# Kernel optimization log

Hardware: AMD Instinct MI355X
Metric: run time of the kernel (lower is better)

The kernel has to match this reference:

```python
import jax, jax.numpy as jnp
import numpy as np
import math

DIM = 768
NUM_HEADS = 16
PERHEAD = DIM // NUM_HEADS  # 48
B, T = 4, 2048


def setup_inputs() -> dict:
    key = jax.random.key(0)
    k_x, k_wi, k_bi, k_wo, k_bo = jax.random.split(key, 5)
    s_in = 1.0 / math.sqrt(DIM)
    return {
        "x": jax.random.normal(k_x, (B, T, DIM), dtype=jnp.float32),
        # linear_in: y = x @ w_in + b_in, w_in: (DIM, 3*DIM)
        "w_in": jax.random.uniform(k_wi, (DIM, 3 * DIM), jnp.float32, -s_in, s_in),
        "b_in": jax.random.uniform(k_bi, (3 * DIM,), jnp.float32, -s_in, s_in),
        "w_out": jax.random.uniform(k_wo, (DIM, DIM), jnp.float32, -s_in, s_in),
        "b_out": jax.random.uniform(k_bo, (DIM,), jnp.float32, -s_in, s_in),
    }


def reference(x, w_in, b_in, w_out, b_out):
    bs, tok, _ = x.shape
    qkv = x @ w_in + b_in                                   # (B, T, 3*DIM)
    # Faithful to torch: reshape to (B, T, H, 3*ph), move heads, chunk last dim.
    qkv = qkv.reshape(bs, tok, NUM_HEADS, 3 * PERHEAD)
    qkv = jnp.transpose(qkv, (0, 2, 1, 3))                  # (B, H, T, 3*ph)
    q, k, v = jnp.split(qkv, 3, axis=-1)                    # each (B, H, T, ph)
    scale = 1.0 / math.sqrt(PERHEAD)
    scores = jnp.einsum("bhqd,bhkd->bhqk", q, k) * scale    # (B, H, T, T)
    attn = jax.nn.softmax(scores, axis=-1)
    # dropout p=0.0 (eval) -> identity
    out = jnp.einsum("bhqk,bhkd->bhqd", attn, v)            # (B, H, T, ph)
    out = jnp.transpose(out, (0, 2, 1, 3)).reshape(bs, tok, DIM)
    return out @ w_out + b_out
```

## Files before the change

kernel.cpp:

```cpp
#include <hip/hip_runtime.h>
#include <hip/hip_bf16.h>
#include <math.h>

typedef __attribute__((ext_vector_type(8))) short short8;
typedef __attribute__((ext_vector_type(4))) float floatx4;
typedef __hip_bfloat16 bf16;

#define DIM 768
#define NHEADS 16
#define PH 48
#define VROWS 49
#define BATCH 4
#define SEQ 2048
#define MTOK (BATCH*SEQ)
#define NQKV (3*DIM)
#define NQK (2*DIM)
#define LOG2E 1.44269504088896f
#define CFAC (0.14433756729740643f * LOG2E)

#define NB_CAST   6144
#define NB_TWIN   1728
#define NB_TWOUT  576
#define NB_MISC   140

__device__ __forceinline__ void cp16(void* dst, const void* src) {
    *(float4*)dst = *(const float4*)src;
}
__device__ __forceinline__ unsigned short f2us(float v) {
    bf16 b = __float2bfloat16(v);
    return *(unsigned short*)&b;
}
__device__ __forceinline__ float us2f(unsigned short u) {
    bf16 b = *(bf16*)&u;
    return __bfloat162float(b);
}
__device__ __forceinline__ void gload_lds16(const bf16* g, bf16* l) {
    __builtin_amdgcn_global_load_lds(
        (const __attribute__((address_space(1))) unsigned int*)g,
        (__attribute__((address_space(3))) unsigned int*)l, 16, 0, 0);
}
__device__ __forceinline__ bool sniff_f32(const unsigned short* __restrict__ x) {
    float v = us2f(x[threadIdx.x & 63]);
    int bad = !(fabsf(v) < 64.0f);
    return __any(bad) != 0;
}

__global__ __launch_bounds__(256) void prep_all(
    const void* __restrict__ x, const void* __restrict__ w_in,
    const void* __restrict__ w_out, const void* __restrict__ bin,
    const void* __restrict__ bout,
    bf16* __restrict__ xb, bf16* __restrict__ winT, bf16* __restrict__ woutT,
    float* __restrict__ bi, float* __restrict__ bo, bf16* __restrict__ Vt)
{
    __shared__ bf16 tile[32][33];
    const int bid = blockIdx.x, tid = threadIdx.x;
    const bool f32 = sniff_f32((const unsigned short*)x);

    if (bid < NB_CAST) {
        int i = bid * 256 + tid;
        if (f32) {
            float4 v = ((const float4*)x)[i];
            ushort4 o;
            o.x = f2us(v.x); o.y = f2us(v.y); o.z = f2us(v.z); o.w = f2us(v.w);
            ((ushort4*)xb)[i] = o;
        } else {
            ((ushort4*)xb)[i] = ((const ushort4*)x)[i];
        }
    } else if (bid < NB_CAST + NB_TWIN + NB_TWOUT) {
        const void* in; bf16* out; int R, C, tt;
        if (bid < NB_CAST + NB_TWIN) {
            in = w_in; out = winT; R = DIM; C = NQKV; tt = bid - NB_CAST;
        } else {
            in = w_out; out = woutT; R = DIM; C = DIM; tt = bid - NB_CAST - NB_TWIN;
        }
        int ctiles = C / 32;
        int c0 = (tt % ctiles) * 32, r0 = (tt / ctiles) * 32;
        int tx = tid & 31, ty = tid >> 5;
#pragma unroll
        for (int j = 0; j < 4; j++) {
            size_t idx = (size_t)(r0 + ty + 8*j) * C + c0 + tx;
            float v = f32 ? ((const float*)in)[idx]
                          : us2f(((const unsigned short*)in)[idx]);
            tile[ty + 8*j][tx] = __float2bfloat16(v);
        }
        __syncthreads();
#pragma unroll
        for (int j = 0; j < 4; j++)
            out[(size_t)(c0 + ty + 8*j) * R + r0 + tx] = tile[tx][ty + 8*j];
    } else {
        int t = (bid - (NB_CAST + NB_TWIN + NB_TWOUT)) * 256 + tid;
        if (t < NQKV) {
            bi[t] = f32 ? ((const float*)bin)[t] : us2f(((const unsigned short*)bin)[t]);
        } else if (t < NQKV + DIM) {
            int j = t - NQKV;
            bo[j] = f32 ? ((const float*)bout)[j] : us2f(((const unsigned short*)bout)[j]);
        } else {
            int k = t - (NQKV + DIM);
            int bh = k >> 9, pos = (k & 511) * 4;
            bf16* dst = Vt + ((size_t)bh * VROWS + 48) * SEQ + pos;
            ushort4 ones;
            ones.x = ones.y = ones.z = ones.w = f2us(1.0f);
            *(ushort4*)dst = ones;
        }
    }
}

template<int N, int MODE, int TM>
__global__ __launch_bounds__(256) void gemm_bias(
    const bf16* __restrict__ A, const bf16* __restrict__ BT,
    const float* __restrict__ bias, void* __restrict__ C0, bf16* __restrict__ Vt,
    const unsigned short* __restrict__ xraw)
{
    constexpr int K = 768;
    constexpr int MI = TM / 32;
    constexpr int TS = TM * 32;
    constexpr int BS = 128 * 32;
    __shared__ __align__(16) bf16 smem[2 * TS + 2 * BS];
    bf16* As0 = smem;
    bf16* As1 = smem + TS;
    bf16* Bs0 = smem + 2 * TS;
    bf16* Bs1 = smem + 2 * TS + BS;
    const bool out_f32 = (MODE == 2) && sniff_f32(xraw);
    const int tid = threadIdx.x;
    const int id = blockIdx.x;
    constexpr int NMB = MTOK / TM;
    const int m0 = (id % NMB) * TM, n0 = (id / NMB) * 128;
    const int w = tid >> 6, lane = tid & 63, lq = lane >> 4, ln = lane & 15;
    const int wr = w & 1, wc = w >> 1;

    const int ssw = ((lane >> 2) ^ (lane >> 4)) & 3;
    const int cm = (lane & 3) ^ ssw;
    const int rlB0 = w * 32 + (lane >> 2), rlB1 = rlB0 + 16;
    const int rlA  = (TM == 128) ? rlB0 : (w * 16 + (lane >> 2));
    const bf16* gA0 = A + (size_t)(m0 + rlA) * K + cm * 8;
    const bf16* gA1 = A + (size_t)(m0 + rlA + ((TM == 128) ? 16 : 0)) * K + cm * 8;
    const bf16* gB0 = BT + (size_t)(n0 + rlB0) * K + cm * 8;
    const bf16* gB1 = BT + (size_t)(n0 + rlB1) * K + cm * 8;
    bf16* lA0 = As0 + ((TM == 128) ? (w * 32) * 32 : (w * 16) * 32);
    bf16* lA1 = As0 + (w * 32 + 16) * 32;
    bf16* lB0 = Bs0 + (w * 32) * 32;
    bf16* lB1 = Bs0 + (w * 32 + 16) * 32;

    const int rsw = (ln ^ (ln >> 2)) & 3;
    const int rchunk = (lq ^ rsw) * 8;

    floatx4 zero4 = {0.f, 0.f, 0.f, 0.f};
    floatx4 acc[MI][4];
#pragma unroll
    for (int mi = 0; mi < MI; mi++)
#pragma unroll
        for (int nj = 0; nj < 4; nj++) acc[mi][nj] = zero4;

    for (int k0 = 0; k0 < K; k0 += 64) {
        gload_lds16(gA0,      lA0);
        gload_lds16(gA0 + 32, lA0 + TS);
        if constexpr (TM == 128) {
            gload_lds16(gA1,      lA1);
            gload_lds16(gA1 + 32, lA1 + TS);
        }
        gload_lds16(gB0,      lB0);
        gload_lds16(gB0 + 32, lB0 + BS);
        gload_lds16(gB1,      lB1);
        gload_lds16(gB1 + 32, lB1 + BS);
        gA0 += 64; gA1 += 64; gB0 += 64; gB1 += 64;
        __syncthreads();

#pragma unroll
        for (int kk = 0; kk < 2; kk++) {
            const bf16* Asub = kk ? As1 : As0;
            const bf16* Bsub = kk ? Bs1 : Bs0;
            short8 a[MI], b[4];
#pragma unroll
            for (int mi = 0; mi < MI; mi++)
                a[mi] = *(const short8*)&Asub[(wr * (TM/2) + 16 * mi + ln) * 32 + rchunk];
#pragma unroll
            for (int nj = 0; nj < 4; nj++)
                b[nj] = *(const short8*)&Bsub[(wc * 64 + 16 * nj + ln) * 32 + rchunk];
#pragma unroll
            for (int mi = 0; mi < MI; mi++)
#pragma unroll
                for (int nj = 0; nj < 4; nj++)
                    acc[mi][nj] = __builtin_amdgcn_mfma_f32_16x16x32_bf16(
                        a[mi], b[nj], acc[mi][nj], 0, 0, 0);
        }
        __syncthreads();
    }
    bf16 (*VLs)[136] = (bf16(*)[136])smem;

#pragma unroll
    for (int nj = 0; nj < 4; nj++) {
        int n = n0 + wc * 64 + 16 * nj + ln;
        float bv = bias[n];
        if (MODE == 2) {
#pragma unroll
            for (int mi = 0; mi < MI; mi++)
#pragma unroll
                for (int i = 0; i < 4; i++) {
                    size_t off = (size_t)(m0 + wr * (TM/2) + 16 * mi + 4 * lq + i) * N + n;
                    float val = acc[mi][nj][i] + bv;
                    if (out_f32) ((float*)C0)[off] = val;
                    else         ((bf16*)C0)[off] = __float2bfloat16(val);
                }
        } else {
            int h = n / 144, r = n - 144 * h;
            if (r < 96) {
                float sc = (r < 48) ? CFAC : 1.0f;
#pragma unroll
                for (int mi = 0; mi < MI; mi++)
#pragma unroll
                    for (int i = 0; i < 4; i++) {
                        size_t off = (size_t)(m0 + wr * (TM/2) + 16 * mi + 4 * lq + i) * NQK
                                     + h * 96 + r;
                        ((bf16*)C0)[off] = __float2bfloat16((acc[mi][nj][i] + bv) * sc);
                    }
            } else {
                int d = r - 96;
#pragma unroll
                for (int mi = 0; mi < MI; mi++)
#pragma unroll
                    for (int i = 0; i < 4; i++)
                        VLs[d][wr * 64 + 32 * (mi >> 1) + 8 * lq + 4 * (mi & 1) + i] =
                            __float2bfloat16(acc[mi][nj][i] + bv);
            }
        }
    }

    if (MODE == 1) {
        __syncthreads();
        const int bidx = m0 >> 11, tok0 = m0 & 2047;
#pragma unroll
        for (int s = 0; s < 3; s++) {
            int idx = tid + 256 * s;
            int d = idx >> 4, ch = idx & 15;
            int h = (n0 + 31 - d) / 144;
            int n = 144 * h + 96 + d;
            if (n >= n0 && n < n0 + 128) {
                bf16* dst = Vt + ((size_t)(bidx * NHEADS + h) * VROWS + d) * SEQ
                            + tok0 + ch * 8;
                *(float4*)dst = *(const float4*)&VLs[d][ch * 8];
            }
        }
    }
}

__global__ __launch_bounds__(256, 2) void attn_fused(
    const bf16* __restrict__ QK, const bf16* __restrict__ Vt, bf16* __restrict__ O)
{
    __shared__ bf16 Ks[2][64][72];
    __shared__ bf16 VsT[2][64][72];

    const int tid = threadIdx.x;
    const int id = blockIdx.x;
    const int g = id & 63, qt = id >> 6;
    const int h = g & 15, b = g >> 4;
    const int w = tid >> 6, lane = tid & 63, lq = lane >> 4, ln = lane & 15;
    const size_t rowbase = (size_t)b * SEQ;
    const int q0 = qt * 256;
    const int hoff = h * 96;
    const bf16* Vth = Vt + (size_t)(b * NHEADS + h) * VROWS * SEQ;

    const bf16 bzero = __float2bfloat16(0.f);
    for (int idx = tid; idx < 2048; idx += 256) {
        int bb = idx >> 10, r = (idx >> 4) & 63, c = idx & 15;
        Ks[bb][r][48 + c] = bzero;
    }

    short8 qa0[4], qa1[4];
    short8 zero8 = {0, 0, 0, 0, 0, 0, 0, 0};
#pragma unroll
    for (int f = 0; f < 4; f++) {
        const bf16* qrow = QK + (rowbase + q0 + 64*f + 16*w + ln) * NQK + hoff;
        qa0[f] = *(const short8*)(qrow + lq * 8);
        qa1[f] = (lq < 2) ? *(const short8*)(qrow + 32 + lq * 8) : zero8;
    }

    const int kr0a = tid / 6, kc0a = tid % 6;
    const int kr1a = (tid + 256) / 6, kc1a = (tid + 256) % 6;
    const char* kg0 = (const char*)(QK + (rowbase + kr0a) * NQK + hoff + 48) + kc0a * 16;
    const char* kg1 = (const char*)(QK + (rowbase + kr1a) * NQK + hoff + 48) + kc1a * 16;
    bf16* kd0 = &Ks[0][kr0a][kc0a * 8];
    bf16* kd1 = &Ks[0][kr1a & 63][kc1a * 8];
    const bool kact = (tid < 128);
    const int vr0 = tid >> 3, vc0 = tid & 7;
    const char* vg0 = (const char*)(Vth + (size_t)vr0 * SEQ) + vc0 * 16;
    const char* vg1 = (const char*)(Vth + (size_t)(32 + vr0) * SEQ) + vc0 * 16;
    bf16* vd0 = &VsT[0][vr0][vc0 * 8];
    bf16* vd1 = &VsT[0][32 + vr0][vc0 * 8];
    const bool vact = (tid < 128);
    const ptrdiff_t KADV = (ptrdiff_t)64 * NQK * 2;
    const ptrdiff_t VADV = 128;
    const int BOFF = 64 * 72;

    floatx4 zero4 = {0.f, 0.f, 0.f, 0.f};
    floatx4 o[4][3];
    float dsum[4] = {0.f, 0.f, 0.f, 0.f};
#pragma unroll
    for (int f = 0; f < 4; f++)
#pragma unroll
        for (int nt = 0; nt < 3; nt++) o[f][nt] = zero4;

    float4 rk0, rk1, rv0, rv1;
    rk0 = *(const float4*)kg0;
    if (kact) rk1 = *(const float4*)kg1;
    rv0 = *(const float4*)vg0;
    if (vact) rv1 = *(const float4*)vg1;
    kg0 += KADV; kg1 += KADV; vg0 += VADV; vg1 += VADV;
    *(float4*)kd0 = rk0;
    if (kact) *(float4*)kd1 = rk1;
    *(float4*)vd0 = rv0;
    if (vact) *(float4*)vd1 = rv1;
    rk0 = *(const float4*)kg0;
    if (kact) rk1 = *(const float4*)kg1;
    rv0 = *(const float4*)vg0;
    if (vact) rv1 = *(const float4*)vg1;
    kg0 += KADV; kg1 += KADV; vg0 += VADV; vg1 += VADV;
    __syncthreads();

    for (int kt = 0; kt < 32; kt++) {
        const int cur = kt & 1;
        if (kt < 31) {
            const int nb = (cur ^ 1) * BOFF;
            *(float4*)(kd0 + nb) = rk0;
            if (kact) *(float4*)(kd1 + nb) = rk1;
            *(float4*)(vd0 + nb) = rv0;
            if (vact) *(float4*)(vd1 + nb) = rv1;
            if (kt < 30) {
                rk0 = *(const float4*)kg0;
                if (kact) rk1 = *(const float4*)kg1;
                rv0 = *(const float4*)vg0;
                if (vact) rv1 = *(const float4*)vg1;
                kg0 += KADV; kg1 += KADV; vg0 += VADV; vg1 += VADV;
            }
        }

        const bf16 (*Kc)[72] = Ks[cur];
        const bf16 (*Vc)[72] = VsT[cur];

        __builtin_amdgcn_s_setprio(1);
        short8 kb0[4], kb1[4];
#pragma unroll
        for (int t = 0; t < 4; t++) {
            kb0[t] = *(const short8*)&Kc[16*t + ln][lq * 8];
            kb1[t] = *(const short8*)&Kc[16*t + ln][lq * 8 + 32];
        }

        short8 pa[4][2];
#pragma unroll
        for (int f = 0; f < 4; f++) {
            floatx4 s[4];
#pragma unroll
            for (int t = 0; t < 4; t++) s[t] = zero4;
#pragma unroll
            for (int t = 0; t < 4; t++) {
                s[t] = __builtin_amdgcn_mfma_f32_16x16x32_bf16(kb0[t], qa0[f], s[t], 0, 0, 0);
                s[t] = __builtin_amdgcn_mfma_f32_16x16x32_bf16(kb1[t], qa1[f], s[t], 0, 0, 0);
            }
#pragma unroll
            for (int ks = 0; ks < 2; ks++) {
                float e0 = __builtin_amdgcn_exp2f(s[2*ks][0]);
                float e1 = __builtin_amdgcn_exp2f(s[2*ks][1]);
                float e2 = __builtin_amdgcn_exp2f(s[2*ks][2]);
                float e3 = __builtin_amdgcn_exp2f(s[2*ks][3]);
                float e4 = __builtin_amdgcn_exp2f(s[2*ks+1][0]);
                float e5 = __builtin_amdgcn_exp2f(s[2*ks+1][1]);
                float e6 = __builtin_amdgcn_exp2f(s[2*ks+1][2]);
                float e7 = __builtin_amdgcn_exp2f(s[2*ks+1][3]);
                dsum[f] += ((e0 + e1) + (e2 + e3)) + ((e4 + e5) + (e6 + e7));
                union { short8 v; __hip_bfloat162 h2[4]; } u;
                float2 p;
                p.x = e0; p.y = e1; u.h2[0] = __float22bfloat162_rn(p);
                p.x = e2; p.y = e3; u.h2[1] = __float22bfloat162_rn(p);
                p.x = e4; p.y = e5; u.h2[2] = __float22bfloat162_rn(p);
                p.x = e6; p.y = e7; u.h2[3] = __float22bfloat162_rn(p);
                pa[f][ks] = u.v;
            }
        }

#pragma unroll
        for (int nt = 0; nt < 3; nt++) {
            short8 vb0 = *(const short8*)&Vc[16*nt + ln][lq * 8];
            short8 vb1 = *(const short8*)&Vc[16*nt + ln][lq * 8 + 32];
#pragma unroll
            for (int f = 0; f < 4; f++) {
                o[f][nt] = __builtin_amdgcn_mfma_f32_16x16x32_bf16(pa[f][0], vb0, o[f][nt], 0, 0, 0);
                o[f][nt] = __builtin_amdgcn_mfma_f32_16x16x32_bf16(pa[f][1], vb1, o[f][nt], 0, 0, 0);
            }
        }
        __builtin_amdgcn_s_setprio(0);
        __syncthreads();
    }

#pragma unroll
    for (int f = 0; f < 4; f++) {
        float dtot = dsum[f];
        dtot += __shfl_xor(dtot, 16);
        dtot += __shfl_xor(dtot, 32);
#pragma unroll
        for (int i = 0; i < 4; i++) {
            float l = __shfl(dtot, 4*lq + i);
            float inv = 1.0f / l;
            int row = q0 + 64*f + 16*w + 4*lq + i;
#pragma unroll
            for (int nt = 0; nt < 3; nt++)
                O[(rowbase + row) * DIM + h * PH + 16*nt + ln] =
                    __float2bfloat16(o[f][nt][i] * inv);
        }
    }
}

extern "C" void kernel_launch(void* const* d_in, const int* in_sizes, int n_in,
                              void* d_out, int out_size, void* d_ws, size_t ws_size,
                              hipStream_t stream) {
    const void* x     = d_in[0];
    const void* w_in  = d_in[1];
    const void* b_in  = d_in[2];
    const void* w_out = d_in[3];
    const void* b_out = d_in[4];

    bf16* qk    = (bf16*)d_ws;
    bf16* Vt    = qk    + (size_t)MTOK * NQK;
    bf16* xb    = Vt    + (size_t)BATCH * NHEADS * VROWS * SEQ;
    bf16* attn  = xb;
    bf16* winT  = xb    + (size_t)MTOK * DIM;
    bf16* woutT = winT  + (size_t)NQKV * DIM;
    float* bi   = (float*)(woutT + (size_t)DIM * DIM);
    float* bo   = bi + NQKV;

    prep_all<<<NB_CAST + NB_TWIN + NB_TWOUT + NB_MISC, 256, 0, stream>>>(
        x, w_in, w_out, b_in, b_out, xb, winT, woutT, bi, bo, Vt);

    gemm_bias<NQKV, 1, 128><<<64 * (NQKV/128), 256, 0, stream>>>(
        xb, winT, bi, qk, Vt, (const unsigned short*)x);
    attn_fused<<<64 * (SEQ/256), 256, 0, stream>>>(qk, Vt, attn);
    gemm_bias<DIM, 2, 64><<<128 * (DIM/128), 256, 0, stream>>>(
        attn, woutT, bo, d_out, nullptr, (const unsigned short*)x);
}
```

Baseline: 215.6 us.

## Load K and V straight into registers, dropping the LDS staging and barriers

After: 263.0 us. 1.22x slower.

```diff
diff --git a/kernel.cpp b/kernel.cpp
--- a/kernel.cpp
+++ b/kernel.cpp
@@ -246,9 +246,6 @@
 __global__ __launch_bounds__(256, 2) void attn_fused(
     const bf16* __restrict__ QK, const bf16* __restrict__ Vt, bf16* __restrict__ O)
 {
-    __shared__ bf16 Ks[2][64][72];
-    __shared__ bf16 VsT[2][64][72];
-
     const int tid = threadIdx.x;
     const int id = blockIdx.x;
     const int g = id & 63, qt = id >> 6;
@@ -259,12 +256,6 @@
     const int hoff = h * 96;
     const bf16* Vth = Vt + (size_t)(b * NHEADS + h) * VROWS * SEQ;
 
-    const bf16 bzero = __float2bfloat16(0.f);
-    for (int idx = tid; idx < 2048; idx += 256) {
-        int bb = idx >> 10, r = (idx >> 4) & 63, c = idx & 15;
-        Ks[bb][r][48 + c] = bzero;
-    }
-
     short8 qa0[4], qa1[4];
     short8 zero8 = {0, 0, 0, 0, 0, 0, 0, 0};
 #pragma unroll
@@ -274,22 +265,8 @@
         qa1[f] = (lq < 2) ? *(const short8*)(qrow + 32 + lq * 8) : zero8;
     }
 
-    const int kr0a = tid / 6, kc0a = tid % 6;
-    const int kr1a = (tid + 256) / 6, kc1a = (tid + 256) % 6;
-    const char* kg0 = (const char*)(QK + (rowbase + kr0a) * NQK + hoff + 48) + kc0a * 16;
-    const char* kg1 = (const char*)(QK + (rowbase + kr1a) * NQK + hoff + 48) + kc1a * 16;
-    bf16* kd0 = &Ks[0][kr0a][kc0a * 8];
-    bf16* kd1 = &Ks[0][kr1a & 63][kc1a * 8];
-    const bool kact = (tid < 128);
-    const int vr0 = tid >> 3, vc0 = tid & 7;
-    const char* vg0 = (const char*)(Vth + (size_t)vr0 * SEQ) + vc0 * 16;
-    const char* vg1 = (const char*)(Vth + (size_t)(32 + vr0) * SEQ) + vc0 * 16;
-    bf16* vd0 = &VsT[0][vr0][vc0 * 8];
-    bf16* vd1 = &VsT[0][32 + vr0][vc0 * 8];
-    const bool vact = (tid < 128);
-    const ptrdiff_t KADV = (ptrdiff_t)64 * NQK * 2;
-    const ptrdiff_t VADV = 128;
-    const int BOFF = 64 * 72;
+    const bf16* kbase = QK + (rowbase + ln) * NQK + hoff + 48 + lq * 8;
+    const bf16* vbase = Vth + (size_t)ln * SEQ + lq * 8;
 
     floatx4 zero4 = {0.f, 0.f, 0.f, 0.f};
     floatx4 o[4][3];
@@ -299,96 +276,70 @@
 #pragma unroll
         for (int nt = 0; nt < 3; nt++) o[f][nt] = zero4;
 
-    float4 rk0, rk1, rv0, rv1;
-    rk0 = *(const float4*)kg0;
-    if (kact) rk1 = *(const float4*)kg1;
-    rv0 = *(const float4*)vg0;
-    if (vact) rv1 = *(const float4*)vg1;
-    kg0 += KADV; kg1 += KADV; vg0 += VADV; vg1 += VADV;
-    *(float4*)kd0 = rk0;
-    if (kact) *(float4*)kd1 = rk1;
-    *(float4*)vd0 = rv0;
-    if (vact) *(float4*)vd1 = rv1;
-    rk0 = *(const float4*)kg0;
-    if (kact) rk1 = *(const float4*)kg1;
-    rv0 = *(const float4*)vg0;
-    if (vact) rv1 = *(const float4*)vg1;
-    kg0 += KADV; kg1 += KADV; vg0 += VADV; vg1 += VADV;
-    __syncthreads();
-
-    for (int kt = 0; kt < 32; kt++) {
-        const int cur = kt & 1;
-        if (kt < 31) {
-            const int nb = (cur ^ 1) * BOFF;
-            *(float4*)(kd0 + nb) = rk0;
-            if (kact) *(float4*)(kd1 + nb) = rk1;
-            *(float4*)(vd0 + nb) = rv0;
-            if (vact) *(float4*)(vd1 + nb) = rv1;
-            if (kt < 30) {
-                rk0 = *(const float4*)kg0;
-                if (kact) rk1 = *(const float4*)kg1;
-                rv0 = *(const float4*)vg0;
-                if (vact) rv1 = *(const float4*)vg1;
-                kg0 += KADV; kg1 += KADV; vg0 += VADV; vg1 += VADV;
-            }
-        }
-
-        const bf16 (*Kc)[72] = Ks[cur];
-        const bf16 (*Vc)[72] = VsT[cur];
-
-        __builtin_amdgcn_s_setprio(1);
-        short8 kb0[4], kb1[4];
-#pragma unroll
-        for (int t = 0; t < 4; t++) {
-            kb0[t] = *(const short8*)&Kc[16*t + ln][lq * 8];
-            kb1[t] = *(const short8*)&Kc[16*t + ln][lq * 8 + 32];
-        }
-
-        short8 pa[4][2];
-#pragma unroll
-        for (int f = 0; f < 4; f++) {
-            floatx4 s[4];
-#pragma unroll
-            for (int t = 0; t < 4; t++) s[t] = zero4;
-#pragma unroll
-            for (int t = 0; t < 4; t++) {
-                s[t] = __builtin_amdgcn_mfma_f32_16x16x32_bf16(kb0[t], qa0[f], s[t], 0, 0, 0);
-                s[t] = __builtin_amdgcn_mfma_f32_16x16x32_bf16(kb1[t], qa1[f], s[t], 0, 0, 0);
-            }
-#pragma unroll
-            for (int ks = 0; ks < 2; ks++) {
-                float e0 = __builtin_amdgcn_exp2f(s[2*ks][0]);
-                float e1 = __builtin_amdgcn_exp2f(s[2*ks][1]);
-                float e2 = __builtin_amdgcn_exp2f(s[2*ks][2]);
-                float e3 = __builtin_amdgcn_exp2f(s[2*ks][3]);
-                float e4 = __builtin_amdgcn_exp2f(s[2*ks+1][0]);
-                float e5 = __builtin_amdgcn_exp2f(s[2*ks+1][1]);
-                float e6 = __builtin_amdgcn_exp2f(s[2*ks+1][2]);
-                float e7 = __builtin_amdgcn_exp2f(s[2*ks+1][3]);
-                dsum[f] += ((e0 + e1) + (e2 + e3)) + ((e4 + e5) + (e6 + e7));
-                union { short8 v; __hip_bfloat162 h2[4]; } u;
-                float2 p;
-                p.x = e0; p.y = e1; u.h2[0] = __float22bfloat162_rn(p);
-                p.x = e2; p.y = e3; u.h2[1] = __float22bfloat162_rn(p);
-                p.x = e4; p.y = e5; u.h2[2] = __float22bfloat162_rn(p);
-                p.x = e6; p.y = e7; u.h2[3] = __float22bfloat162_rn(p);
-                pa[f][ks] = u.v;
-            }
-        }
-
-#pragma unroll
-        for (int nt = 0; nt < 3; nt++) {
-            short8 vb0 = *(const short8*)&Vc[16*nt + ln][lq * 8];
-            short8 vb1 = *(const short8*)&Vc[16*nt + ln][lq * 8 + 32];
-#pragma unroll
-            for (int f = 0; f < 4; f++) {
-                o[f][nt] = __builtin_amdgcn_mfma_f32_16x16x32_bf16(pa[f][0], vb0, o[f][nt], 0, 0, 0);
-                o[f][nt] = __builtin_amdgcn_mfma_f32_16x16x32_bf16(pa[f][1], vb1, o[f][nt], 0, 0, 0);
-            }
-        }
-        __builtin_amdgcn_s_setprio(0);
-        __syncthreads();
-    }
+    short8 k0A[4], k1A[4], k0B[4], k1B[4];
+
+#define LOADK(d0, d1, ktt) do {                                              \
+    _Pragma("unroll")                                                        \
+    for (int t = 0; t < 4; t++) {                                            \
+        const bf16* kp = kbase + (size_t)((ktt) * 64 + 16 * t) * NQK;        \
+        d0[t] = *(const short8*)kp;                                          \
+        d1[t] = *(const short8*)(kp + 32);                                   \
+    } } while (0)
+
+#define STEP(c0, c1, ktt) do {                                               \
+    short8 vb[3][2];                                                         \
+    _Pragma("unroll")                                                        \
+    for (int nt = 0; nt < 3; nt++) {                                         \
+        const bf16* vp = vbase + (size_t)(16 * nt) * SEQ + (ktt) * 64;       \
+        vb[nt][0] = *(const short8*)vp;                                      \
+        vb[nt][1] = *(const short8*)(vp + 32);                               \
+    }                                                                        \
+    _Pragma("unroll")                                                        \
+    for (int f = 0; f < 4; f++) {                                            \
+        floatx4 s[4];                                                        \
+        _Pragma("unroll")                                                    \
+        for (int t = 0; t < 4; t++) {                                        \
+            s[t] = zero4;                                                    \
+            s[t] = __builtin_amdgcn_mfma_f32_16x16x32_bf16(c0[t], qa0[f], s[t], 0, 0, 0); \
+            s[t] = __builtin_amdgcn_mfma_f32_16x16x32_bf16(c1[t], qa1[f], s[t], 0, 0, 0); \
+        }                                                                    \
+        short8 pa0, pa1;                                                     \
+        _Pragma("unroll")                                                    \
+        for (int ks = 0; ks < 2; ks++) {                                     \
+            float e0 = __builtin_amdgcn_exp2f(s[2*ks][0]);                   \
+            float e1 = __builtin_amdgcn_exp2f(s[2*ks][1]);                   \
+            float e2 = __builtin_amdgcn_exp2f(s[2*ks][2]);                   \
+            float e3 = __builtin_amdgcn_exp2f(s[2*ks][3]);                   \
+            float e4 = __builtin_amdgcn_exp2f(s[2*ks+1][0]);                 \
+            float e5 = __builtin_amdgcn_exp2f(s[2*ks+1][1]);                 \
+            float e6 = __builtin_amdgcn_exp2f(s[2*ks+1][2]);                 \
+            float e7 = __builtin_amdgcn_exp2f(s[2*ks+1][3]);                 \
+            dsum[f] += ((e0 + e1) + (e2 + e3)) + ((e4 + e5) + (e6 + e7));    \
+            union { short8 v; __hip_bfloat162 h2[4]; } u;                    \
+            float2 p;                                                        \
+            p.x = e0; p.y = e1; u.h2[0] = __float22bfloat162_rn(p);          \
+            p.x = e2; p.y = e3; u.h2[1] = __float22bfloat162_rn(p);          \
+            p.x = e4; p.y = e5; u.h2[2] = __float22bfloat162_rn(p);          \
+            p.x = e6; p.y = e7; u.h2[3] = __float22bfloat162_rn(p);          \
+            if (ks == 0) pa0 = u.v; else pa1 = u.v;                          \
+        }                                                                    \
+        _Pragma("unroll")                                                    \
+        for (int nt = 0; nt < 3; nt++) {                                     \
+            o[f][nt] = __builtin_amdgcn_mfma_f32_16x16x32_bf16(pa0, vb[nt][0], o[f][nt], 0, 0, 0); \
+            o[f][nt] = __builtin_amdgcn_mfma_f32_16x16x32_bf16(pa1, vb[nt][1], o[f][nt], 0, 0, 0); \
+        }                                                                    \
+    } } while (0)
+
+    LOADK(k0A, k1A, 0);
+    for (int kt = 0; kt < 32; kt += 2) {
+        LOADK(k0B, k1B, kt + 1);
+        STEP(k0A, k1A, kt);
+        if (kt < 30)
+            LOADK(k0A, k1A, kt + 2);
+        STEP(k0B, k1B, kt + 1);
+    }
+#undef LOADK
+#undef STEP
 
 #pragma unroll
     for (int f = 0; f < 4; f++) {
```
